# Optimization experiments

Measured on AMD Instinct MI355X. Metric: run time of the kernel, lower is better.

## Reference

```python
import jax, jax.numpy as jnp
import numpy as np

# dims: batch, support_size(K), query_len(total_Q*max_len), hidden; num_tags(N), max_len
B, S, TQ, D = 4, 16, 2048, 768
NT, ML = 64, 1
NK = S * NT                # == N*K*max_len == 1024
MID1 = int(NK * ML / 5)    # 204 (torch int(1/5*N*K*max_len))
MID2 = int(TQ * ML / 5)    # 409 (torch int(1/5*total_Q*max_len))


def _mlp(x, w1, b1, w2, b2):
    return jax.nn.relu(x @ w1 + b1) @ w2 + b2


def setup_inputs() -> dict:
    key = jax.random.key(0)
    ks = jax.random.split(key, 10)
    w = lambda k, shape: jax.random.normal(k, shape, jnp.float32) * 0.02
    labels = jax.random.randint(ks[2], (B, S, ML), 0, NT)
    return dict(
        test_reps=jax.random.normal(ks[0], (B, S, TQ, D), jnp.float32),
        support_reps=jax.random.normal(ks[1], (B, S, ML, D), jnp.float32),
        test_output_mask=jnp.ones((B, TQ), jnp.int32),
        support_output_mask=jnp.ones((B, S, ML), jnp.int32),
        support_targets=jax.nn.one_hot(labels, NT, dtype=jnp.float32),
        l1_w1=w(ks[3], (NK * ML, MID1)), l1_b1=jnp.zeros((MID1,), jnp.float32),
        l1_w2=w(ks[4], (MID1, NK * ML)), l1_b2=jnp.zeros((NK * ML,), jnp.float32),
        l2_w1=w(ks[5], (TQ * ML, MID2)), l2_b1=jnp.zeros((MID2,), jnp.float32),
        l2_w2=w(ks[6], (MID2, TQ * ML)), l2_b2=jnp.zeros((TQ * ML,), jnp.float32),
        fu_w1=w(ks[7], (2 * ML, ML)), fu_b1=jnp.zeros((ML,), jnp.float32),
        fu_w2=w(ks[8], (ML, ML)), fu_b2=jnp.zeros((ML,), jnp.float32),
    )


def reference(test_reps, support_reps, test_output_mask, support_output_mask,
              support_targets, l1_w1, l1_b1, l1_w2, l1_b2,
              l2_w1, l2_b1, l2_w2, l2_b2, fu_w1, fu_b1, fu_w2, fu_b2):
    b, s, tq, d = test_reps.shape
    ml = support_reps.shape[2]
    nt = support_targets.shape[-1]
    # mean over support copies of query reps -> (B, TQ, D)
    test = test_reps.mean(axis=1)
    tgt = support_targets.astype(test.dtype)
    # per-support-example tag-summed reps: (B, S, NT, D)
    sum_reps = jnp.einsum('bstn,bstd->bsnd', tgt, support_reps)
    support = sum_reps.reshape(b, s * nt, d)          # (B, NK*ML, D)
    # cross similarity matrix
    W = jnp.einsum('bnd,bqd->bnq', support, test)     # (B, NK, TQ)
    # branch 1: pool over query axis, MLP, -> weights over support rows
    W1m = _mlp(W.max(axis=2), l1_w1, l1_b1, l1_w2, l1_b2).reshape(b, -1, ml)
    W1a = _mlp(W.mean(axis=2), l1_w1, l1_b1, l1_w2, l1_b2).reshape(b, -1, ml)
    W1 = _mlp(jnp.concatenate([W1a, W1m], axis=-1), fu_w1, fu_b1, fu_w2, fu_b2)
    # branch 2: pool over support axis, MLP, -> weights over query tokens
    W2m = _mlp(W.max(axis=1), l2_w1, l2_b1, l2_w2, l2_b2).reshape(b, -1, ml)
    W2a = _mlp(W.mean(axis=1), l2_w1, l2_b1, l2_w2, l2_b2).reshape(b, -1, ml)
    W2 = _mlp(jnp.concatenate([W2a, W2m], axis=-1), fu_w1, fu_b1, fu_w2, fu_b2)
    W1 = jax.nn.softmax(W1, axis=1) + 1.0
    W2 = jax.nn.softmax(W2, axis=1) + 1.0
    # weighted sums over the max_len axis
    sup_w = (W1[..., None] * support.reshape(b, -1, ml, d)).sum(axis=2)  # (B, S*NT, D)
    qry_w = (W2[..., None] * test.reshape(b, -1, ml, d)).sum(axis=2)     # (B, TQ, D)
    # prototypes averaged by tag counts
    sum2 = sup_w.reshape(b, s, nt, d).sum(axis=1)                        # (B, NT, D)
    tag_count = tgt.reshape(b, -1, nt).sum(axis=1)[..., None] + 1e-4     # remove_0
    proto = sum2 / tag_count
    sim = jnp.einsum('bqd,bnd->bqn', qry_w, proto)                       # (B, TQ, NT)
    return sim, proto
```

## Files before the change

kernel.cpp:

```cpp
#include <hip/hip_runtime.h>
#include <hip/hip_bf16.h>
#include <float.h>
#include <math.h>

#define BB   4
#define SS   16
#define TQN  2048
#define DD   768
#define NTT  64
#define NKK  1024
#define MID1 204
#define MID2 409

typedef float nt_f4 __attribute__((ext_vector_type(4)));

__global__ __launch_bounds__(192) void k_mean_u(const nt_f4* __restrict__ reps,
                                                const float4* __restrict__ sup,
                                                float* __restrict__ U) {
    const int QD4 = TQN * DD / 4;
    int bq = blockIdx.x;
    int b = bq >> 11, q = bq & 2047;
    int t = threadIdx.x;
    const nt_f4* base = reps + ((size_t)b * SS * TQN + q) * (DD / 4) + t;
    nt_f4 acc = {0.f, 0.f, 0.f, 0.f};
#pragma unroll
    for (int s = 0; s < SS; ++s)
        acc += base[(size_t)s * QD4];
    acc *= (1.f / SS);
    float4 av; av.x = acc.x; av.y = acc.y; av.z = acc.z; av.w = acc.w;

    float part[SS];
#pragma unroll
    for (int s = 0; s < SS; ++s) {
        float4 sv = sup[((size_t)b * SS + s) * (DD / 4) + t];
        part[s] = av.x * sv.x + av.y * sv.y + av.z * sv.z + av.w * sv.w;
    }
    __shared__ float rbuf[3][SS];
    int lane = t & 63, wv = t >> 6;
#pragma unroll
    for (int s = 0; s < SS; ++s) {
        float v = part[s];
        for (int o = 32; o; o >>= 1) v += __shfl_down(v, o, 64);
        if (lane == 0) rbuf[wv][s] = v;
    }
    __syncthreads();
    if (t < SS)
        U[((size_t)b * SS + t) * TQN + q] = rbuf[0][t] + rbuf[1][t] + rbuf[2][t];
}

__global__ __launch_bounds__(256) void k_stats(const float* __restrict__ U,
                                               const float* __restrict__ tgt,
                                               float* __restrict__ Umax, float* __restrict__ Umin,
                                               float* __restrict__ Usum,
                                               float* __restrict__ cmax, float* __restrict__ cmin,
                                               float* __restrict__ csum) {
    int bs = blockIdx.x, t = threadIdx.x;
    const float* u = U + (size_t)bs * TQN;
    float mx = -FLT_MAX, mn = FLT_MAX, sm = 0.f;
#pragma unroll
    for (int k = 0; k < TQN / 256; ++k) {
        float v = u[t + 256 * k];
        mx = fmaxf(mx, v); mn = fminf(mn, v); sm += v;
    }
    int lane = t & 63, wv = t >> 6;
    for (int o = 32; o; o >>= 1) {
        mx = fmaxf(mx, __shfl_down(mx, o, 64));
        mn = fminf(mn, __shfl_down(mn, o, 64));
        sm += __shfl_down(sm, o, 64);
    }
    __shared__ float smx[4], smn[4], ssm[4];
    if (lane == 0) { smx[wv] = mx; smn[wv] = mn; ssm[wv] = sm; }
    __syncthreads();
    if (t == 0) {
        Umax[bs] = fmaxf(fmaxf(smx[0], smx[1]), fmaxf(smx[2], smx[3]));
        Umin[bs] = fminf(fminf(smn[0], smn[1]), fminf(smn[2], smn[3]));
        Usum[bs] = ssm[0] + ssm[1] + ssm[2] + ssm[3];
    }
    if (wv == 1) {
        float v = tgt[(size_t)bs * NTT + lane];
        float tmx = v, tmn = v, tsm = v;
        for (int o = 32; o; o >>= 1) {
            tmx = fmaxf(tmx, __shfl_down(tmx, o, 64));
            tmn = fminf(tmn, __shfl_down(tmn, o, 64));
            tsm += __shfl_down(tsm, o, 64);
        }
        if (lane == 0) { cmax[bs] = tmx; cmin[bs] = tmn; csum[bs] = tsm; }
    }
}

__global__ __launch_bounds__(256) void k_feat(const float* __restrict__ tgt,
                                              const float* __restrict__ Umax,
                                              const float* __restrict__ Umin,
                                              const float* __restrict__ Usum,
                                              const float* __restrict__ U,
                                              const float* __restrict__ cmax,
                                              const float* __restrict__ cmin,
                                              const float* __restrict__ csum,
                                              float* __restrict__ xm1, float* __restrict__ xa1,
                                              float* __restrict__ xm2, float* __restrict__ xa2) {
    int i = blockIdx.x * 256 + threadIdx.x;
    if (i < BB * NKK) {
        int b = i >> 10, bs = b * SS + ((i & 1023) >> 6);
        float c = tgt[i];
        xm1[i] = c > 0.f ? c * Umax[bs] : (c < 0.f ? c * Umin[bs] : 0.f);
        xa1[i] = c * Usum[bs] * (1.f / TQN);
    } else {
        int i2 = i - BB * NKK;
        if (i2 < BB * TQN) {
            int b = i2 >> 11, q = i2 & 2047;
            float vmax = -FLT_MAX, vsum = 0.f;
#pragma unroll
            for (int s = 0; s < SS; ++s) {
                int bs = b * SS + s;
                float u = U[(size_t)bs * TQN + q];
                float pm_ = u > 0.f ? u * cmax[bs] : (u < 0.f ? u * cmin[bs] : 0.f);
                vmax = fmaxf(vmax, pm_);
                vsum += u * csum[bs];
            }
            xm2[i2] = vmax;
            xa2[i2] = vsum * (1.f / NKK);
        }
    }
}

template<int NH, int JT, int RC>
__device__ __forceinline__ void h_body(int b, int jt, int rc, int t,
                                       const float* __restrict__ xm,
                                       const float* __restrict__ xa,
                                       const float* __restrict__ w1,
                                       float* __restrict__ pm_, float* __restrict__ pa_,
                                       float* sxm, float* sxa) {
    int rbase = rc * 256;
    sxm[t] = xm[rbase + t];
    sxa[t] = xa[rbase + t];
    __syncthreads();
    int lane = t & 63, wv = t >> 6;
    int j = jt * 64 + lane;
    float accm = 0.f, acca = 0.f;
    if (j < NH) {
        const float* wp = w1 + (size_t)(rbase + wv * 64) * NH + j;
#pragma unroll
        for (int rr = 0; rr < 64; ++rr) {
            float w = wp[(size_t)rr * NH];
            accm += sxm[wv * 64 + rr] * w;
            acca += sxa[wv * 64 + rr] * w;
        }
    }
    __shared__ float pm[4][64], pa[4][64];
    pm[wv][lane] = accm; pa[wv][lane] = acca;
    __syncthreads();
    if (t < 64) {
        int idx = ((b * JT + jt) * RC + rc) * 64 + t;
        pm_[idx] = pm[0][t] + pm[1][t] + pm[2][t] + pm[3][t];
        pa_[idx] = pa[0][t] + pa[1][t] + pa[2][t] + pa[3][t];
    }
}

__global__ __launch_bounds__(256) void k_hA(const float* __restrict__ xm1,
                                            const float* __restrict__ xa1,
                                            const float* __restrict__ xm2,
                                            const float* __restrict__ xa2,
                                            const float* __restrict__ w1a,
                                            const float* __restrict__ w1b,
                                            float* __restrict__ p1m, float* __restrict__ p1a,
                                            float* __restrict__ p2m, float* __restrict__ p2a) {
    __shared__ float sxm[256], sxa[256];
    int blk = blockIdx.x, t = threadIdx.x;
    if (blk < 64) {
        int b = blk >> 4, jt = (blk >> 2) & 3, rc = blk & 3;
        h_body<MID1, 4, 4>(b, jt, rc, t, xm1 + b * NKK, xa1 + b * NKK, w1a,
                           p1m, p1a, sxm, sxa);
    } else {
        int blk2 = blk - 64;
        int b = blk2 / 56, r_ = blk2 % 56, jt = r_ >> 3, rc = r_ & 7;
        h_body<MID2, 7, 8>(b, jt, rc, t, xm2 + b * TQN, xa2 + b * TQN, w1b,
                           p2m, p2a, sxm, sxa);
    }
}

template<int NH, int NOUT, int RT, int JC, int CHJ, int JT, int RC>
__device__ __forceinline__ void o_body(int b, int rt, int jc, int t,
                                       const float* __restrict__ pmL,
                                       const float* __restrict__ paL,
                                       const float* __restrict__ b1,
                                       const float* __restrict__ w2,
                                       float* __restrict__ qm_, float* __restrict__ qa_,
                                       float* shm, float* sha) {
    int jbase = jc * CHJ;
    if (t < CHJ) {
        int j = jbase + t;
        if (j < NH) {
            int jt_ = j >> 6, t64 = j & 63;
            float m_ = 0.f, a_ = 0.f;
#pragma unroll
            for (int rc = 0; rc < RC; ++rc) {
                int idx = ((b * JT + jt_) * RC + rc) * 64 + t64;
                m_ += pmL[idx]; a_ += paL[idx];
            }
            float bb_ = b1[j];
            shm[t] = fmaxf(m_ + bb_, 0.f);
            sha[t] = fmaxf(a_ + bb_, 0.f);
        } else { shm[t] = 0.f; sha[t] = 0.f; }
    }
    __syncthreads();
    int rl = t & 127, jp = t >> 7;
    int r = rt * 128 + rl;
    float accm = 0.f, acca = 0.f;
#pragma unroll 8
    for (int jj = jp; jj < CHJ; jj += 2) {
        int j = jbase + jj;
        int j2 = j < NH ? j : NH - 1;
        float w = w2[(size_t)j2 * NOUT + r];
        accm += shm[jj] * w; acca += sha[jj] * w;
    }
    __shared__ float qm[2][128], qa[2][128];
    qm[jp][rl] = accm; qa[jp][rl] = acca;
    __syncthreads();
    if (t < 128) {
        int idx = ((b * RT + rt) * JC + jc) * 128 + t;
        qm_[idx] = qm[0][t] + qm[1][t];
        qa_[idx] = qa[0][t] + qa[1][t];
    }
}

__global__ __launch_bounds__(256) void k_oA(const float* __restrict__ p1m,
                                            const float* __restrict__ p1a,
                                            const float* __restrict__ p2m,
                                            const float* __restrict__ p2a,
                                            const float* __restrict__ b1a_,
                                            const float* __restrict__ b1b_,
                                            const float* __restrict__ w2a,
                                            const float* __restrict__ w2b,
                                            float* __restrict__ q1m, float* __restrict__ q1a,
                                            float* __restrict__ q2m, float* __restrict__ q2a) {
    __shared__ float shm[104], sha[104];
    int blk = blockIdx.x, t = threadIdx.x;
    if (blk < 64) {
        int b = blk >> 4, rt = (blk >> 1) & 7, jc = blk & 1;
        o_body<MID1, NKK, 8, 2, 102, 4, 4>(b, rt, jc, t, p1m, p1a, b1a_, w2a,
                                           q1m, q1a, shm, sha);
    } else {
        int blk2 = blk - 64;
        int b = blk2 >> 6, r_ = blk2 & 63, rt = r_ >> 2, jc = r_ & 3;
        o_body<MID2, TQN, 16, 4, 103, 7, 8>(b, rt, jc, t, p2m, p2a, b1b_, w2b,
                                            q2m, q2a, shm, sha);
    }
}

__global__ __launch_bounds__(256) void k_smx(const float* __restrict__ q1m,
                                             const float* __restrict__ q1a,
                                             const float* __restrict__ q2m,
                                             const float* __restrict__ q2a,
                                             const float* __restrict__ b2a_,
                                             const float* __restrict__ b2b_,
                                             const float* __restrict__ fw1, const float* __restrict__ fb1,
                                             const float* __restrict__ fw2, const float* __restrict__ fb2,
                                             float* __restrict__ W1, float* __restrict__ W2) {
    int blk = blockIdx.x, t = threadIdx.x;
    int lane = t & 63, wv = t >> 6;
    float f0 = fw1[0], f1 = fw1[1], fb = fb1[0], g0 = fw2[0], gb = fb2[0];
    __shared__ float rb[4];

    if (blk < BB) {
        int b = blk;
        float yv[4];
#pragma unroll
        for (int k = 0; k < 4; ++k) {
            int r = t + 256 * k;
            int rt = r >> 7, rl = r & 127;
            float bb_ = b2a_[r];
            float ym = bb_, ya = bb_;
#pragma unroll
            for (int jc = 0; jc < 2; ++jc) {
                int idx = ((b * 8 + rt) * 2 + jc) * 128 + rl;
                ym += q1m[idx]; ya += q1a[idx];
            }
            float z = fmaxf(ya * f0 + ym * f1 + fb, 0.f);
            yv[k] = z * g0 + gb;
        }
        float mx = fmaxf(fmaxf(yv[0], yv[1]), fmaxf(yv[2], yv[3]));
        for (int o = 32; o; o >>= 1) mx = fmaxf(mx, __shfl_down(mx, o, 64));
        if (lane == 0) rb[wv] = mx;
        __syncthreads();
        mx = fmaxf(fmaxf(rb[0], rb[1]), fmaxf(rb[2], rb[3]));
        __syncthreads();
        float e[4], sm = 0.f;
#pragma unroll
        for (int k = 0; k < 4; ++k) { e[k] = expf(yv[k] - mx); sm += e[k]; }
        for (int o = 32; o; o >>= 1) sm += __shfl_down(sm, o, 64);
        if (lane == 0) rb[wv] = sm;
        __syncthreads();
        sm = rb[0] + rb[1] + rb[2] + rb[3];
        float inv = 1.f / sm;
#pragma unroll
        for (int k = 0; k < 4; ++k)
            W1[b * NKK + t + 256 * k] = e[k] * inv + 1.f;
    } else {
        int b = blk - BB;
        float yv[8];
#pragma unroll
        for (int k = 0; k < 8; ++k) {
            int r = t + 256 * k;
            int rt = r >> 7, rl = r & 127;
            float bb_ = b2b_[r];
            float ym = bb_, ya = bb_;
#pragma unroll
            for (int jc = 0; jc < 4; ++jc) {
                int idx = ((b * 16 + rt) * 4 + jc) * 128 + rl;
                ym += q2m[idx]; ya += q2a[idx];
            }
            float z = fmaxf(ya * f0 + ym * f1 + fb, 0.f);
            yv[k] = z * g0 + gb;
        }
        float mx = yv[0];
#pragma unroll
        for (int k = 1; k < 8; ++k) mx = fmaxf(mx, yv[k]);
        for (int o = 32; o; o >>= 1) mx = fmaxf(mx, __shfl_down(mx, o, 64));
        if (lane == 0) rb[wv] = mx;
        __syncthreads();
        mx = fmaxf(fmaxf(rb[0], rb[1]), fmaxf(rb[2], rb[3]));
        __syncthreads();
        float e[8], sm = 0.f;
#pragma unroll
        for (int k = 0; k < 8; ++k) { e[k] = expf(yv[k] - mx); sm += e[k]; }
        for (int o = 32; o; o >>= 1) sm += __shfl_down(sm, o, 64);
        if (lane == 0) rb[wv] = sm;
        __syncthreads();
        sm = rb[0] + rb[1] + rb[2] + rb[3];
        float inv = 1.f / sm;
#pragma unroll
        for (int k = 0; k < 8; ++k) W2[b * TQN + t + 256 * k] = e[k] * inv + 1.f;
    }
}

__global__ __launch_bounds__(256) void k_proto(const float* __restrict__ W1,
                                               const float* __restrict__ tgt,
                                               const float* __restrict__ sup,
                                               float* __restrict__ proto,
                                               float* __restrict__ c2) {
    int bn = blockIdx.x;
    int b = bn >> 6, n = bn & 63;
    int t = threadIdx.x;
    float a0 = 0.f, a1 = 0.f, a2 = 0.f, cnt = 0.f;
#pragma unroll
    for (int s = 0; s < SS; ++s) {
        float tg = tgt[((size_t)b * SS + s) * NTT + n];
        float coef = W1[b * NKK + s * NTT + n] * tg;
        const float* sv = sup + ((size_t)b * SS + s) * DD;
        a0 += coef * sv[t];
        a1 += coef * sv[t + 256];
        a2 += coef * sv[t + 512];
        cnt += tg;
    }
    float inv = 1.f / (cnt + 1e-4f);
    float* p = proto + (size_t)bn * DD;
    p[t] = a0 * inv; p[t + 256] = a1 * inv; p[t + 512] = a2 * inv;
    if (t < SS) {
        float tg = tgt[((size_t)b * SS + t) * NTT + n];
        c2[((size_t)b * SS + t) * NTT + n] = W1[b * NKK + t * NTT + n] * tg * inv;
    }
}

__global__ __launch_bounds__(256) void k_simU(const float* __restrict__ U,
                                              const float* __restrict__ c2,
                                              const float* __restrict__ W2,
                                              float* __restrict__ sim) {
    int blk = blockIdx.x;
    int b = blk >> 3, q0 = (blk & 7) * 256;
    int t = threadIdx.x;
    __shared__ float sc[SS][NTT];
    for (int i = t; i < SS * NTT; i += 256)
        sc[i >> 6][i & 63] = c2[(size_t)b * SS * NTT + i];
    __syncthreads();
    int q = q0 + t;
    float u[SS];
#pragma unroll
    for (int s = 0; s < SS; ++s)
        u[s] = U[((size_t)b * SS + s) * TQN + q];
    float w = W2[b * TQN + q];
    float* simp = sim + ((size_t)b * TQN + q) * NTT;
#pragma unroll 4
    for (int n4 = 0; n4 < NTT / 4; ++n4) {
        float4 o;
        float a0 = 0.f, a1 = 0.f, a2 = 0.f, a3 = 0.f;
#pragma unroll
        for (int s = 0; s < SS; ++s) {
            float us = u[s];
            a0 += us * sc[s][n4 * 4 + 0];
            a1 += us * sc[s][n4 * 4 + 1];
            a2 += us * sc[s][n4 * 4 + 2];
            a3 += us * sc[s][n4 * 4 + 3];
        }
        o.x = a0 * w; o.y = a1 * w; o.z = a2 * w; o.w = a3 * w;
        *reinterpret_cast<float4*>(&simp[n4 * 4]) = o;
    }
}

extern "C" void kernel_launch(void* const* d_in, const int* in_sizes, int n_in,
                              void* d_out, int out_size, void* d_ws, size_t ws_size,
                              hipStream_t stream) {
    const float* reps = (const float*)d_in[0];
    const float* sup  = (const float*)d_in[1];
    const float* tgt  = (const float*)d_in[4];
    const float* l1w1 = (const float*)d_in[5];
    const float* l1b1 = (const float*)d_in[6];
    const float* l1w2 = (const float*)d_in[7];
    const float* l1b2 = (const float*)d_in[8];
    const float* l2w1 = (const float*)d_in[9];
    const float* l2b1 = (const float*)d_in[10];
    const float* l2w2 = (const float*)d_in[11];
    const float* l2b2 = (const float*)d_in[12];
    const float* fw1  = (const float*)d_in[13];
    const float* fb1  = (const float*)d_in[14];
    const float* fw2  = (const float*)d_in[15];
    const float* fb2  = (const float*)d_in[16];

    float* out    = (float*)d_out;
    float* simO   = out;
    float* protoO = out + (size_t)BB * TQN * NTT;

    float* w = (float*)d_ws;
    float* U     = w; w += (size_t)BB * SS * TQN;
    float* Umax  = w; w += 64;
    float* Umin  = w; w += 64;
    float* Usum  = w; w += 64;
    float* cmaxp = w; w += 64;
    float* cminp = w; w += 64;
    float* csump = w; w += 64;
    float* xm1   = w; w += BB * NKK;
    float* xa1   = w; w += BB * NKK;
    float* xm2   = w; w += BB * TQN;
    float* xa2   = w; w += BB * TQN;
    float* p1m   = w; w += BB * 4 * 4 * 64;
    float* p1a   = w; w += BB * 4 * 4 * 64;
    float* p2m   = w; w += BB * 7 * 8 * 64;
    float* p2a   = w; w += BB * 7 * 8 * 64;
    float* q1m   = w; w += BB * 8 * 2 * 128;
    float* q1a   = w; w += BB * 8 * 2 * 128;
    float* q2m   = w; w += BB * 16 * 4 * 128;
    float* q2a   = w; w += BB * 16 * 4 * 128;
    float* W1    = w; w += BB * NKK;
    float* W2    = w; w += BB * TQN;
    float* c2    = w; w += BB * SS * NTT;

    k_mean_u<<<BB * TQN, 192, 0, stream>>>((const nt_f4*)reps, (const float4*)sup, U);
    k_stats<<<BB * SS, 256, 0, stream>>>(U, tgt, Umax, Umin, Usum, cmaxp, cminp, csump);
    k_feat<<<(BB * NKK + BB * TQN) / 256, 256, 0, stream>>>(tgt, Umax, Umin, Usum,
                                                            U, cmaxp, cminp, csump,
                                                            xm1, xa1, xm2, xa2);
    k_hA<<<64 + 224, 256, 0, stream>>>(xm1, xa1, xm2, xa2, l1w1, l2w1,
                                       p1m, p1a, p2m, p2a);
    k_oA<<<64 + 256, 256, 0, stream>>>(p1m, p1a, p2m, p2a, l1b1, l2b1,
                                       l1w2, l2w2, q1m, q1a, q2m, q2a);
    k_smx<<<2 * BB, 256, 0, stream>>>(q1m, q1a, q2m, q2a, l1b2, l2b2,
                                      fw1, fb1, fw2, fb2, W1, W2);
    k_proto<<<BB * NTT, 256, 0, stream>>>(W1, tgt, sup, protoO, c2);
    k_simU<<<BB * (TQN / 256), 256, 0, stream>>>(U, c2, W2, simO);
}
```

Before: 127.8 us.

## Process eight queries per block in k_mean_u with support staged in LDS

The mean-and-project kernel now handles 8 query rows per 256-thread block, with each 32-thread group owning one query, instead of one query per 192-thread block. The block's 16 support vectors are loaded once into shared memory and reused across the 8 queries, replacing repeated global reads, and reductions shrink to 32-lane shuffles with no cross-wave shared-memory step. This cuts global support traffic and the reduction and sync overhead per query, at the cost of 48 KB of LDS per block, which may limit occupancy on a kernel bound by reading the large reps tensor.

```diff
diff --git a/kernel.cpp b/kernel.cpp
--- a/kernel.cpp
+++ b/kernel.cpp
@@ -14,38 +14,45 @@
 
 typedef float nt_f4 __attribute__((ext_vector_type(4)));
 
-__global__ __launch_bounds__(192) void k_mean_u(const nt_f4* __restrict__ reps,
+__global__ __launch_bounds__(256) void k_mean_u(const nt_f4* __restrict__ reps,
                                                 const float4* __restrict__ sup,
                                                 float* __restrict__ U) {
-    const int QD4 = TQN * DD / 4;
-    int bq = blockIdx.x;
-    int b = bq >> 11, q = bq & 2047;
+    const int QD4 = DD / 4;
+    int blk = blockIdx.x;
+    int b = blk >> 8, q0 = (blk & 255) * 8;
     int t = threadIdx.x;
-    const nt_f4* base = reps + ((size_t)b * SS * TQN + q) * (DD / 4) + t;
-    nt_f4 acc = {0.f, 0.f, 0.f, 0.f};
-#pragma unroll
-    for (int s = 0; s < SS; ++s)
-        acc += base[(size_t)s * QD4];
-    acc *= (1.f / SS);
-    float4 av; av.x = acc.x; av.y = acc.y; av.z = acc.z; av.w = acc.w;
-
-    float part[SS];
-#pragma unroll
+    int ql = t >> 5;
+    int qb = t & 31;
+
+    __shared__ float4 ssup[SS * QD4];
+    for (int i = t; i < SS * QD4; i += 256)
+        ssup[i] = sup[(size_t)b * SS * QD4 + i];
+
+    nt_f4 acc[6] = {};
+    const nt_f4* base = reps + ((size_t)b * SS * TQN + q0 + ql) * QD4;
+    const size_t sstr = (size_t)TQN * QD4;
     for (int s = 0; s < SS; ++s) {
-        float4 sv = sup[((size_t)b * SS + s) * (DD / 4) + t];
-        part[s] = av.x * sv.x + av.y * sv.y + av.z * sv.z + av.w * sv.w;
-    }
-    __shared__ float rbuf[3][SS];
-    int lane = t & 63, wv = t >> 6;
-#pragma unroll
+        const nt_f4* p = base + (size_t)s * sstr;
+#pragma unroll
+        for (int k = 0; k < 6; ++k)
+            acc[k] += p[qb + 32 * k];
+    }
+#pragma unroll
+    for (int k = 0; k < 6; ++k) acc[k] *= (1.f / SS);
+    __syncthreads();
+
     for (int s = 0; s < SS; ++s) {
-        float v = part[s];
-        for (int o = 32; o; o >>= 1) v += __shfl_down(v, o, 64);
-        if (lane == 0) rbuf[wv][s] = v;
-    }
-    __syncthreads();
-    if (t < SS)
-        U[((size_t)b * SS + t) * TQN + q] = rbuf[0][t] + rbuf[1][t] + rbuf[2][t];
+        float psum = 0.f;
+#pragma unroll
+        for (int k = 0; k < 6; ++k) {
+            float4 sv = ssup[s * QD4 + qb + 32 * k];
+            psum += acc[k].x * sv.x + acc[k].y * sv.y
+                  + acc[k].z * sv.z + acc[k].w * sv.w;
+        }
+        for (int o = 16; o; o >>= 1) psum += __shfl_down(psum, o, 32);
+        if (qb == 0)
+            U[((size_t)(b * SS + s)) * TQN + q0 + ql] = psum;
+    }
 }
 
 __global__ __launch_bounds__(256) void k_stats(const float* __restrict__ U,
@@ -443,7 +450,8 @@
     float* W2    = w; w += BB * TQN;
     float* c2    = w; w += BB * SS * NTT;
 
-    k_mean_u<<<BB * TQN, 192, 0, stream>>>((const nt_f4*)reps, (const float4*)sup, U);
+    k_mean_u<<<BB * (TQN / 8), 256, 0, stream>>>((const nt_f4*)reps,
+                                                 (const float4*)sup, U);
     k_stats<<<BB * SS, 256, 0, stream>>>(U, tgt, Umax, Umin, Usum, cmaxp, cminp, csump);
     k_feat<<<(BB * NKK + BB * TQN) / 256, 256, 0, stream>>>(tgt, Umax, Umin, Usum,
                                                             U, cmaxp, cminp, csump,
```

New measurement: 122.1 us (median of 2 runs). -4.5%, faster.
